# Kernel tuning notes

Measured on AMD Instinct MI355X. Metric: run time of the kernel, lower is better.

Reference implementation:

```python
import jax, jax.numpy as jnp
import numpy as np

LEVEL = 256
BLOCKS = 8
THRESH = 10.0


def setup_inputs() -> dict:
    key = jax.random.key(0)
    img = jax.random.randint(key, (16, 1024, 1024), 0, LEVEL).astype(jnp.float32)
    return {"img": img}


def _clahe(img):
    B, H, W = img.shape
    bm, bn = H // BLOCKS, W // BLOCKS
    v = img.astype(jnp.int32)  # pixel values 0..255, used as histogram bins

    # ---- per-block histograms via one flat scatter-add (segment_sum) ----
    bi = jnp.arange(H) // bm                      # block row per pixel row
    bj = jnp.arange(W) // bn                      # block col per pixel col
    blk = bi[:, None] * BLOCKS + bj[None, :]      # [H, W] block id
    seg = (jnp.arange(B)[:, None, None] * (BLOCKS * BLOCKS) + blk[None]) * LEVEL + v
    hists = jax.ops.segment_sum(
        jnp.ones((B * H * W,), jnp.float32), seg.reshape(-1),
        num_segments=B * BLOCKS * BLOCKS * LEVEL)
    hists = hists.reshape(B, BLOCKS, BLOCKS, LEVEL)

    # ---- clip histogram: redistribute excess above threshold uniformly ----
    # threshold_value = sum(hists)/LEVEL*threshold ; block sum is bm*bn exactly
    tv = (bm * bn) / LEVEL * THRESH
    total_extra = jnp.sum(jnp.maximum(hists - tv, 0.0), axis=-1, keepdims=True)
    mean_extra = total_extra / LEVEL
    # int() truncation of non-negative values == floor
    clip = jnp.floor(jnp.where(hists >= tv, tv + mean_extra, hists + mean_extra))

    # ---- CDF -> uint8 mapping table per block ----
    cdf = jnp.cumsum(clip, axis=-1) * ((LEVEL - 1) / (bm * bn))
    maps = (jnp.floor(cdf).astype(jnp.int32) % 256).astype(jnp.float32)  # [B,BLOCKS,BLOCKS,LEVEL]

    # ---- per-pixel bilinear blend of 2x2 neighboring block maps ----
    ii = jnp.arange(H, dtype=jnp.float32)
    jj = jnp.arange(W, dtype=jnp.float32)
    # Python int() truncates toward zero, so r,c are always >= 0
    r = jnp.trunc((ii - bm / 2) / bm).astype(jnp.int32)   # [H]
    c = jnp.trunc((jj - bn / 2) / bn).astype(jnp.int32)   # [W]
    x1 = (ii - (r.astype(jnp.float32) + 0.5) * bm) / bm   # [H]
    y1 = (jj - (c.astype(jnp.float32) + 0.5) * bn) / bn   # [W]
    rp = jnp.minimum(r + 1, BLOCKS - 1)
    cp = jnp.minimum(c + 1, BLOCKS - 1)
    # on last block row/col the original falls back to 1-D / nearest interp:
    x1e = jnp.where(r >= BLOCKS - 1, 0.0, x1)[:, None]    # [H,1]
    y1e = jnp.where(c >= BLOCKS - 1, 0.0, y1)[None, :]    # [1,W]

    bidx = jnp.arange(B)[:, None, None]

    def gather(rr, cc):  # maps[b, rr[i], cc[j], v[b,i,j]] -> [B,H,W]
        return maps[bidx, rr[None, :, None], cc[None, None, :], v]

    lu = gather(r, c)
    lb = gather(rp, c)
    ru = gather(r, cp)
    rb = gather(rp, cp)
    out = (1 - y1e) * ((1 - x1e) * lu + x1e * lb) + y1e * ((1 - x1e) * ru + x1e * rb)
    # final .astype('uint8') cast
    return (jnp.trunc(out).astype(jnp.int32) % 256).astype(jnp.float32)


def reference(img) -> jnp.ndarray:
    return _clahe(img)
```

## Files before the change

### kernel.cpp

```cpp
#include <hip/hip_runtime.h>
#include <hip/hip_bf16.h>

#define LEVEL 256
#define BLOCKS 8

__global__ __launch_bounds__(256) void clahe_hist_kernel(const float* __restrict__ img,
                                                         float* __restrict__ maps,
                                                         unsigned char* __restrict__ u8img) {
    __shared__ int   hist[256];
    __shared__ float red[256];
    __shared__ float scan[256];
    __shared__ float s_me;

    const int t   = threadIdx.x;
    const int bid = blockIdx.x;
    const int b   = bid >> 6;
    const int blk = bid & 63;
    const int br  = blk >> 3;
    const int bc  = blk & 7;

    hist[t] = 0;
    __syncthreads();

    const size_t base = (size_t)b * 1048576 + (size_t)(br * 128) * 1024 + (size_t)(bc * 128);
    const float* p = img + base;
    unsigned char* q8 = u8img ? (u8img + base) : nullptr;
    for (int it = 0; it < 16; ++it) {
        int idx = it * 256 + t;
        int y   = idx >> 5;
        int x   = (idx & 31) * 4;
        float4 v = *(const float4*)(p + (size_t)y * 1024 + x);
        int va = (int)v.x, vb = (int)v.y, vc = (int)v.z, vd = (int)v.w;
        atomicAdd(&hist[va], 1);
        atomicAdd(&hist[vb], 1);
        atomicAdd(&hist[vc], 1);
        atomicAdd(&hist[vd], 1);
        if (q8) {
            uchar4 pk;
            pk.x = (unsigned char)va; pk.y = (unsigned char)vb;
            pk.z = (unsigned char)vc; pk.w = (unsigned char)vd;
            *(uchar4*)(q8 + (size_t)y * 1024 + x) = pk;
        }
    }
    __syncthreads();

    const float tv = 640.0f;
    float h = (float)hist[t];
    float extra = fmaxf(h - tv, 0.0f);
    red[t] = extra;
    __syncthreads();
    for (int off = 128; off > 0; off >>= 1) {
        if (t < off) red[t] += red[t + off];
        __syncthreads();
    }
    if (t == 0) s_me = red[0] * (1.0f / 256.0f);
    __syncthreads();
    const float me = s_me;
    float clip = floorf(((h >= tv) ? tv : h) + me);

    scan[t] = clip;
    __syncthreads();
    for (int off = 1; off < 256; off <<= 1) {
        float add = (t >= off) ? scan[t - off] : 0.0f;
        __syncthreads();
        scan[t] += add;
        __syncthreads();
    }
    float cdf = scan[t] * (255.0f / 16384.0f);
    int m = ((int)floorf(cdf)) & 255;
    maps[(size_t)bid * 256 + t] = (float)m;
}

template <bool U8>
__global__ __launch_bounds__(256) void clahe_map_kernel(const float* __restrict__ imgf,
                                                        const unsigned char* __restrict__ img8,
                                                        const float* __restrict__ maps,
                                                        float* __restrict__ out) {
#pragma clang fp contract(off)
    __shared__ float4 m4[256];

    const int t  = threadIdx.x;
    const int b  = blockIdx.z;
    const int i0 = blockIdx.y * 64;
    const int j0 = blockIdx.x * 64;

    const int r  = (i0 >= 64) ? ((i0 - 64) >> 7) : 0;
    const int c  = (j0 >= 64) ? ((j0 - 64) >> 7) : 0;
    const int rp = min(r + 1, BLOCKS - 1);
    const int cp = min(c + 1, BLOCKS - 1);
    const bool rEdge = (r >= BLOCKS - 1);
    const bool cEdge = (c >= BLOCKS - 1);

    const float* mb = maps + (size_t)b * 64 * 256;
    {
        float lu = mb[(r  * 8 + c ) * 256 + t];
        float lb = mb[(rp * 8 + c ) * 256 + t];
        float ru = mb[(r  * 8 + cp) * 256 + t];
        float rb = mb[(rp * 8 + cp) * 256 + t];
        m4[t] = make_float4(lu, lb, ru, rb);
    }
    __syncthreads();

    const size_t ibase = (size_t)b * 1048576;
    const int row_in = t >> 4;
    const int col4   = (t & 15) * 4;

    for (int it = 0; it < 4; ++it) {
        const int i = i0 + it * 16 + row_in;
        const int j = j0 + col4;

        int vv[4];
        if (U8) {
            uchar4 px = *(const uchar4*)(img8 + ibase + (size_t)i * 1024 + j);
            vv[0] = px.x; vv[1] = px.y; vv[2] = px.z; vv[3] = px.w;
        } else {
            float4 px = *(const float4*)(imgf + ibase + (size_t)i * 1024 + j);
            vv[0] = (int)px.x; vv[1] = (int)px.y; vv[2] = (int)px.z; vv[3] = (int)px.w;
        }

        const float x1  = rEdge ? 0.0f : ((float)i - (float)(r * 128 + 64)) * 0.0078125f;
        const float x0  = 1.0f - x1;

        float4 o4;
        float* ov = (float*)&o4;
        for (int k = 0; k < 4; ++k) {
            const int jj = j + k;
            const float y1 = cEdge ? 0.0f : ((float)jj - (float)(c * 128 + 64)) * 0.0078125f;
            const float4 q = m4[vv[k]];
            float o = (1.0f - y1) * (x0 * q.x + x1 * q.y)
                    + y1 * (x0 * q.z + x1 * q.w);
            ov[k] = (float)(((int)o) & 255);
        }
        *(float4*)(out + ibase + (size_t)i * 1024 + j) = o4;
    }
}

extern "C" void kernel_launch(void* const* d_in, const int* in_sizes, int n_in,
                              void* d_out, int out_size, void* d_ws, size_t ws_size,
                              hipStream_t stream) {
    const float* img = (const float*)d_in[0];
    float* out = (float*)d_out;
    float* maps = (float*)d_ws;

    const size_t maps_bytes = (size_t)1024 * 256 * sizeof(float);
    const size_t u8_bytes   = (size_t)16 * 1024 * 1024;
    const bool use_u8 = ws_size >= maps_bytes + u8_bytes;
    unsigned char* u8img = use_u8 ? ((unsigned char*)d_ws + maps_bytes) : nullptr;

    clahe_hist_kernel<<<dim3(1024), dim3(256), 0, stream>>>(img, maps, u8img);
    if (use_u8) {
        clahe_map_kernel<true><<<dim3(16, 16, 16), dim3(256), 0, stream>>>(
            nullptr, u8img, maps, out);
    } else {
        clahe_map_kernel<false><<<dim3(16, 16, 16), dim3(256), 0, stream>>>(
            img, nullptr, maps, out);
    }
}
```

Measured before the change: 124.0 us.

## Fuse histogram and mapping into one cooperative kernel keeping pixels in registers

Replaces the two-kernel pipeline with a single cooperative kernel of 512 workgroups. Each workgroup builds histograms and maps for two tiles, synchronizes the whole grid, then interpolates its own tiles using pixel values kept packed in registers. This removes the second read of the image (or of the u8 copy) and the u8 write. The lookup table is also packed into 4 bytes per entry instead of a float4 to cut LDS traffic. It risks grid-sync overhead and register pressure from holding 32 packed words per thread, and falls back to the old path if the cooperative launch fails.

```diff
diff --git a/kernel.cpp b/kernel.cpp
--- a/kernel.cpp
+++ b/kernel.cpp
@@ -1,8 +1,143 @@
 #include <hip/hip_runtime.h>
 #include <hip/hip_bf16.h>
+#include <hip/hip_cooperative_groups.h>
+
+namespace cg = cooperative_groups;
 
 #define LEVEL 256
 #define BLOCKS 8
+
+__global__ __launch_bounds__(256, 4) void clahe_fused(const float* __restrict__ img,
+                                                      float* __restrict__ out,
+                                                      float* __restrict__ maps) {
+#pragma clang fp contract(off)
+    __shared__ int   hist[256];
+    __shared__ float red[256];
+    __shared__ float scan[256];
+    __shared__ float s_me;
+    __shared__ unsigned int tbl[4][256];
+
+    const int t = threadIdx.x;
+    unsigned int pix[2][16];
+
+    for (int g = 0; g < 2; ++g) {
+        const int bid = blockIdx.x * 2 + g;
+        const int b   = bid >> 6;
+        const int blk = bid & 63;
+        const int br  = blk >> 3;
+        const int bc  = blk & 7;
+
+        hist[t] = 0;
+        __syncthreads();
+
+        const size_t base = (size_t)b * 1048576 + (size_t)(br * 128) * 1024 + (size_t)(bc * 128);
+        const float* p = img + base;
+#pragma unroll
+        for (int it = 0; it < 16; ++it) {
+            int idx = it * 256 + t;
+            int y   = idx >> 5;
+            int x   = (idx & 31) * 4;
+            float4 v = *(const float4*)(p + (size_t)y * 1024 + x);
+            int va = (int)v.x, vb = (int)v.y, vc = (int)v.z, vd = (int)v.w;
+            atomicAdd(&hist[va], 1);
+            atomicAdd(&hist[vb], 1);
+            atomicAdd(&hist[vc], 1);
+            atomicAdd(&hist[vd], 1);
+            pix[g][it] = (unsigned)va | ((unsigned)vb << 8) |
+                         ((unsigned)vc << 16) | ((unsigned)vd << 24);
+        }
+        __syncthreads();
+
+        const float tv = 640.0f;
+        float h = (float)hist[t];
+        red[t] = fmaxf(h - tv, 0.0f);
+        __syncthreads();
+        for (int off = 128; off > 0; off >>= 1) {
+            if (t < off) red[t] += red[t + off];
+            __syncthreads();
+        }
+        if (t == 0) s_me = red[0] * (1.0f / 256.0f);
+        __syncthreads();
+        const float me = s_me;
+        float clip = floorf(((h >= tv) ? tv : h) + me);
+
+        scan[t] = clip;
+        __syncthreads();
+        for (int off = 1; off < 256; off <<= 1) {
+            float add = (t >= off) ? scan[t - off] : 0.0f;
+            __syncthreads();
+            scan[t] += add;
+            __syncthreads();
+        }
+        float cdf = scan[t] * (255.0f / 16384.0f);
+        maps[(size_t)bid * 256 + t] = (float)(((int)floorf(cdf)) & 255);
+        __syncthreads();
+    }
+
+    __threadfence();
+    cg::this_grid().sync();
+
+    for (int g = 0; g < 2; ++g) {
+        const int bid = blockIdx.x * 2 + g;
+        const int b   = bid >> 6;
+        const int blk = bid & 63;
+        const int br  = blk >> 3;
+        const int bc  = blk & 7;
+        const float* mb = maps + (size_t)b * 64 * 256;
+
+        __syncthreads();
+#pragma unroll
+        for (int q = 0; q < 4; ++q) {
+            int qi = q >> 1, qj = q & 1;
+            int i0 = br * 128 + qi * 64;
+            int j0 = bc * 128 + qj * 64;
+            int r  = (i0 >= 64) ? ((i0 - 64) >> 7) : 0;
+            int c  = (j0 >= 64) ? ((j0 - 64) >> 7) : 0;
+            int rp = min(r + 1, BLOCKS - 1);
+            int cp = min(c + 1, BLOCKS - 1);
+            unsigned lu = (unsigned)(int)mb[(r  * 8 + c ) * 256 + t];
+            unsigned lb = (unsigned)(int)mb[(rp * 8 + c ) * 256 + t];
+            unsigned ru = (unsigned)(int)mb[(r  * 8 + cp) * 256 + t];
+            unsigned rb = (unsigned)(int)mb[(rp * 8 + cp) * 256 + t];
+            tbl[q][t] = lu | (lb << 8) | (ru << 16) | (rb << 24);
+        }
+        __syncthreads();
+
+        const size_t base = (size_t)b * 1048576 + (size_t)(br * 128) * 1024 + (size_t)(bc * 128);
+        float* po = out + base;
+#pragma unroll
+        for (int it = 0; it < 16; ++it) {
+            int idx = it * 256 + t;
+            int y   = idx >> 5;
+            int x   = (idx & 31) * 4;
+            int i   = br * 128 + y;
+            int q   = ((y >> 6) << 1) | (x >> 6);
+
+            int   r  = (i >= 64) ? ((i - 64) >> 7) : 0;
+            float x1 = (r >= BLOCKS - 1) ? 0.0f : (float)(i - (r * 128 + 64)) * 0.0078125f;
+            float x0 = 1.0f - x1;
+
+            unsigned w = pix[g][it];
+            float4 o4;
+            float* ov = (float*)&o4;
+#pragma unroll
+            for (int k = 0; k < 4; ++k) {
+                int jj = bc * 128 + x + k;
+                int cc = (jj >= 64) ? ((jj - 64) >> 7) : 0;
+                float y1 = (cc >= BLOCKS - 1) ? 0.0f : (float)(jj - (cc * 128 + 64)) * 0.0078125f;
+                unsigned mv = tbl[q][(w >> (k * 8)) & 255u];
+                float lu = (float)(mv & 255u);
+                float lb = (float)((mv >> 8) & 255u);
+                float ru = (float)((mv >> 16) & 255u);
+                float rb = (float)(mv >> 24);
+                float o = (1.0f - y1) * (x0 * lu + x1 * lb)
+                        + y1 * (x0 * ru + x1 * rb);
+                ov[k] = (float)(((int)o) & 255);
+            }
+            *(float4*)(po + (size_t)y * 1024 + x) = o4;
+        }
+    }
+}
 
 __global__ __launch_bounds__(256) void clahe_hist_kernel(const float* __restrict__ img,
                                                          float* __restrict__ maps,
@@ -46,8 +181,7 @@
 
     const float tv = 640.0f;
     float h = (float)hist[t];
-    float extra = fmaxf(h - tv, 0.0f);
-    red[t] = extra;
+    red[t] = fmaxf(h - tv, 0.0f);
     __syncthreads();
     for (int off = 128; off > 0; off >>= 1) {
         if (t < off) red[t] += red[t + off];
@@ -67,8 +201,7 @@
         __syncthreads();
     }
     float cdf = scan[t] * (255.0f / 16384.0f);
-    int m = ((int)floorf(cdf)) & 255;
-    maps[(size_t)bid * 256 + t] = (float)m;
+    maps[(size_t)bid * 256 + t] = (float)(((int)floorf(cdf)) & 255);
 }
 
 template <bool U8>
@@ -77,7 +210,7 @@
                                                         const float* __restrict__ maps,
                                                         float* __restrict__ out) {
 #pragma clang fp contract(off)
-    __shared__ float4 m4[256];
+    __shared__ unsigned int tbl[256];
 
     const int t  = threadIdx.x;
     const int b  = blockIdx.z;
@@ -93,11 +226,11 @@
 
     const float* mb = maps + (size_t)b * 64 * 256;
     {
-        float lu = mb[(r  * 8 + c ) * 256 + t];
-        float lb = mb[(rp * 8 + c ) * 256 + t];
-        float ru = mb[(r  * 8 + cp) * 256 + t];
-        float rb = mb[(rp * 8 + cp) * 256 + t];
-        m4[t] = make_float4(lu, lb, ru, rb);
+        unsigned lu = (unsigned)(int)mb[(r  * 8 + c ) * 256 + t];
+        unsigned lb = (unsigned)(int)mb[(rp * 8 + c ) * 256 + t];
+        unsigned ru = (unsigned)(int)mb[(r  * 8 + cp) * 256 + t];
+        unsigned rb = (unsigned)(int)mb[(rp * 8 + cp) * 256 + t];
+        tbl[t] = lu | (lb << 8) | (ru << 16) | (rb << 24);
     }
     __syncthreads();
 
@@ -118,17 +251,21 @@
             vv[0] = (int)px.x; vv[1] = (int)px.y; vv[2] = (int)px.z; vv[3] = (int)px.w;
         }
 
-        const float x1  = rEdge ? 0.0f : ((float)i - (float)(r * 128 + 64)) * 0.0078125f;
-        const float x0  = 1.0f - x1;
+        const float x1 = rEdge ? 0.0f : ((float)i - (float)(r * 128 + 64)) * 0.0078125f;
+        const float x0 = 1.0f - x1;
 
         float4 o4;
         float* ov = (float*)&o4;
         for (int k = 0; k < 4; ++k) {
             const int jj = j + k;
             const float y1 = cEdge ? 0.0f : ((float)jj - (float)(c * 128 + 64)) * 0.0078125f;
-            const float4 q = m4[vv[k]];
-            float o = (1.0f - y1) * (x0 * q.x + x1 * q.y)
-                    + y1 * (x0 * q.z + x1 * q.w);
+            unsigned mv = tbl[vv[k]];
+            float lu = (float)(mv & 255u);
+            float lb = (float)((mv >> 8) & 255u);
+            float ru = (float)((mv >> 16) & 255u);
+            float rb = (float)(mv >> 24);
+            float o = (1.0f - y1) * (x0 * lu + x1 * lb)
+                    + y1 * (x0 * ru + x1 * rb);
             ov[k] = (float)(((int)o) & 255);
         }
         *(float4*)(out + ibase + (size_t)i * 1024 + j) = o4;
@@ -139,20 +276,25 @@
                               void* d_out, int out_size, void* d_ws, size_t ws_size,
                               hipStream_t stream) {
     const float* img = (const float*)d_in[0];
-    float* out = (float*)d_out;
+    float* out  = (float*)d_out;
     float* maps = (float*)d_ws;
 
-    const size_t maps_bytes = (size_t)1024 * 256 * sizeof(float);
-    const size_t u8_bytes   = (size_t)16 * 1024 * 1024;
-    const bool use_u8 = ws_size >= maps_bytes + u8_bytes;
-    unsigned char* u8img = use_u8 ? ((unsigned char*)d_ws + maps_bytes) : nullptr;
-
-    clahe_hist_kernel<<<dim3(1024), dim3(256), 0, stream>>>(img, maps, u8img);
-    if (use_u8) {
-        clahe_map_kernel<true><<<dim3(16, 16, 16), dim3(256), 0, stream>>>(
-            nullptr, u8img, maps, out);
-    } else {
-        clahe_map_kernel<false><<<dim3(16, 16, 16), dim3(256), 0, stream>>>(
-            img, nullptr, maps, out);
+    void* args[] = { (void*)&img, (void*)&out, (void*)&maps };
+    hipError_t err = hipLaunchCooperativeKernel((const void*)clahe_fused,
+                                                dim3(512), dim3(256), args, 0, stream);
+    if (err != hipSuccess) {
+        const size_t maps_bytes = (size_t)1024 * 256 * sizeof(float);
+        const size_t u8_bytes   = (size_t)16 * 1024 * 1024;
+        const bool use_u8 = ws_size >= maps_bytes + u8_bytes;
+        unsigned char* u8img = use_u8 ? ((unsigned char*)d_ws + maps_bytes) : nullptr;
+
+        clahe_hist_kernel<<<dim3(1024), dim3(256), 0, stream>>>(img, maps, u8img);
+        if (use_u8) {
+            clahe_map_kernel<true><<<dim3(16, 16, 16), dim3(256), 0, stream>>>(
+                nullptr, u8img, maps, out);
+        } else {
+            clahe_map_kernel<false><<<dim3(16, 16, 16), dim3(256), 0, stream>>>(
+                img, nullptr, maps, out);
+        }
     }
 }
```

After: 239.2 us. +92.9%, slower.
